# Kernel tuning notes

Hardware: AMD Instinct MI355X
Metric: run time of the kernel (lower is better)

The kernel has to match this reference:

```python
import jax, jax.numpy as jnp
import numpy as np

B, T, I, H, O = 256, 512, 128, 512, 64
ALPHA = 0.2          # cfg.leak
BETA = 8.0           # cfg.softplus_beta
THRESH = 20.0        # cfg.softplus_threshold


def _phi(x):
    # F.softplus(x, beta, threshold): linear when beta*x > threshold
    z = BETA * x
    return jnp.where(z > THRESH, x, jax.nn.softplus(jnp.minimum(z, THRESH)) / BETA)


def setup_inputs() -> dict:
    key = jax.random.key(0)
    ks = jax.random.split(key, 6)
    x = jax.random.normal(ks[0], (B, T, I), dtype=jnp.float32)
    W_xh = jax.random.normal(ks[1], (H, I), dtype=jnp.float32) * (1.0 / np.sqrt(I))
    # E/I structure: column-wise sign (abs weights * sign), scaled to modest spectral radius
    sign = np.ones(H, dtype=np.float32)
    perm = np.random.default_rng(0).permutation(H)
    sign[perm[int(round(0.8 * H)):]] = -1.0
    W_hh = jnp.abs(jax.random.normal(ks[2], (H, H), dtype=jnp.float32)) * jnp.asarray(sign)[None, :]
    W_hh = W_hh * (1.2 / (jnp.linalg.norm(W_hh, ord=2) + 1e-6))
    b_h = jnp.zeros((H,), dtype=jnp.float32)
    W_out = jax.random.normal(ks[3], (O, H), dtype=jnp.float32) * (1.0 / np.sqrt(H))
    b_out = jnp.zeros((O,), dtype=jnp.float32)
    return {"x": x, "W_xh": W_xh, "W_hh": W_hh, "b_h": b_h, "W_out": W_out, "b_out": b_out}


def reference(x, W_xh, W_hh, b_h, W_out, b_out):
    # precompute input projection: [B,T,H]
    xw = jnp.einsum('bti,hi->bth', x, W_xh)

    def step(h, xw_t):  # h: [B,H], xw_t: [B,H]
        pre = xw_t + h @ W_hh.T + b_h
        h = (1.0 - ALPHA) * h + ALPHA * _phi(pre)
        y = h @ W_out.T + b_out  # readout='all'
        return h, y

    h0 = jnp.zeros((x.shape[0], W_hh.shape[0]), dtype=x.dtype)
    _, ys = jax.lax.scan(step, h0, jnp.swapaxes(xw, 0, 1))  # ys: [T,B,O]
    return jnp.swapaxes(ys, 0, 1)  # [B,T,O]
```

## Files before the change

kernel.cpp:

```cpp
#include <hip/hip_runtime.h>


#define BB 256
#define TT 512
#define II 128
#define HH 512
#define OO 64
#define RG 16
#define JC 64
#define NG 16
#define NC 8
#define NB (NG * NC)

typedef _Float16 f16;
typedef f16 f16x8 __attribute__((ext_vector_type(8)));
typedef float f32x4 __attribute__((ext_vector_type(4)));

__global__ __launch_bounds__(256, 1)
void eirnn_persist(const float* __restrict__ x,
                   const float* __restrict__ Wxh,
                   const float* __restrict__ Whh,
                   const float* __restrict__ bh,
                   const float* __restrict__ Wout,
                   const float* __restrict__ bout,
                   float* __restrict__ yout,
                   unsigned long long* __restrict__ hbuf)
{
    const int tid  = threadIdx.x;
    const int bid  = blockIdx.x;
    const int wave = tid >> 6;
    const int lane = tid & 63;
    const int quad = lane >> 4;
    const int l16  = lane & 15;
    const int mm   = bid >> 3;
    const int c    = mm >> 1;
    const int r    = (bid & 7) * 2 + (mm & 1);
    const int rowbase = r * RG;
    const int jbase   = c * JC;
    const int myrow   = wave * 16 + l16;

    __shared__ __align__(16) f16 hg[2][RG][HH + 8];
    __shared__ __align__(16) f16 xsh[2][RG][II + 8];

    f16x8 bf[16];
    f16x8 xbf[4];
    f16x8 bfo[2];
    {
        const float* wp = Whh + (size_t)(jbase + myrow) * HH + quad * 8;
        #pragma unroll
        for (int ks = 0; ks < 16; ++ks) {
            float4 u = *(const float4*)(wp + ks * 32);
            float4 v = *(const float4*)(wp + ks * 32 + 4);
            f16x8 tv;
            tv[0]=(f16)u.x; tv[1]=(f16)u.y; tv[2]=(f16)u.z; tv[3]=(f16)u.w;
            tv[4]=(f16)v.x; tv[5]=(f16)v.y; tv[6]=(f16)v.z; tv[7]=(f16)v.w;
            bf[ks] = tv;
        }
        const float* wq = Wxh + (size_t)(jbase + myrow) * II + quad * 8;
        #pragma unroll
        for (int ks = 0; ks < 4; ++ks) {
            float4 u = *(const float4*)(wq + ks * 32);
            float4 v = *(const float4*)(wq + ks * 32 + 4);
            f16x8 tv;
            tv[0]=(f16)u.x; tv[1]=(f16)u.y; tv[2]=(f16)u.z; tv[3]=(f16)u.w;
            tv[4]=(f16)v.x; tv[5]=(f16)v.y; tv[6]=(f16)v.z; tv[7]=(f16)v.w;
            xbf[ks] = tv;
        }
        const float* wo = Wout + (size_t)myrow * HH + c * 64 + quad * 8;
        #pragma unroll
        for (int ks = 0; ks < 2; ++ks) {
            float4 u = *(const float4*)(wo + ks * 32);
            float4 v = *(const float4*)(wo + ks * 32 + 4);
            f16x8 tv;
            tv[0]=(f16)u.x; tv[1]=(f16)u.y; tv[2]=(f16)u.z; tv[3]=(f16)u.w;
            tv[4]=(f16)v.x; tv[5]=(f16)v.y; tv[6]=(f16)v.z; tv[7]=(f16)v.w;
            bfo[ks] = tv;
        }
    }
    const float biash = bh[jbase + myrow];
    const float biaso = (c == 0) ? bout[myrow] : 0.0f;

    for (int p = tid; p < RG * (HH + 8); p += 256)
        ((unsigned int*)hg)[p] = 0u;

    float hreg[4] = {0.f, 0.f, 0.f, 0.f};

    const int j8     = tid;
    const int gshard = j8 >> 5;

    float4 xpf0, xpf1;
    {
        int p0 = tid, p1 = tid + 256;
        xpf0 = ((const float4*)(x + ((size_t)(rowbase + (p0 >> 5)) * TT + 0) * II))[p0 & 31];
        xpf1 = ((const float4*)(x + ((size_t)(rowbase + (p1 >> 5)) * TT + 0) * II))[p1 & 31];
    }

    __syncthreads();

    for (int t = 0; t <= TT; ++t) {
        const int pcur = t & 1;

        if (t < TT) {
            int p0 = tid, p1 = tid + 256;
            f16* d0 = &xsh[pcur][p0 >> 5][(p0 & 31) * 4];
            d0[0]=(f16)xpf0.x; d0[1]=(f16)xpf0.y; d0[2]=(f16)xpf0.z; d0[3]=(f16)xpf0.w;
            f16* d1 = &xsh[pcur][p1 >> 5][(p1 & 31) * 4];
            d1[0]=(f16)xpf1.x; d1[1]=(f16)xpf1.y; d1[2]=(f16)xpf1.z; d1[3]=(f16)xpf1.w;
        }
        if (t + 1 < TT) {
            int p0 = tid, p1 = tid + 256;
            xpf0 = ((const float4*)(x + ((size_t)(rowbase + (p0 >> 5)) * TT + (t + 1)) * II))[p0 & 31];
            xpf1 = ((const float4*)(x + ((size_t)(rowbase + (p1 >> 5)) * TT + (t + 1)) * II))[p1 & 31];
        }
        if (t >= 1 && gshard != c) {
            const unsigned long long* src = hbuf
                + (size_t)pcur * (BB * HH / 2)
                + (size_t)rowbase * (HH / 2) + j8;
            const unsigned int tg = (unsigned)t;
            unsigned long long v0, v1, v2, v3, v4, v5, v6, v7;
            unsigned long long v8, v9, v10, v11, v12, v13, v14, v15;
            int round = 0;
            for (;;) {
                if ((round & 3) != 3) {
                    asm volatile(
                        "global_load_dwordx2 %0, %8, off sc0\n\t"
                        "global_load_dwordx2 %1, %9, off sc0\n\t"
                        "global_load_dwordx2 %2, %10, off sc0\n\t"
                        "global_load_dwordx2 %3, %11, off sc0\n\t"
                        "global_load_dwordx2 %4, %12, off sc0\n\t"
                        "global_load_dwordx2 %5, %13, off sc0\n\t"
                        "global_load_dwordx2 %6, %14, off sc0\n\t"
                        "global_load_dwordx2 %7, %15, off sc0"
                        : "=&v"(v0), "=&v"(v1), "=&v"(v2), "=&v"(v3),
                          "=&v"(v4), "=&v"(v5), "=&v"(v6), "=&v"(v7)
                        : "v"((unsigned long long)(src)),
                          "v"((unsigned long long)(src + 1 * (HH / 2))),
                          "v"((unsigned long long)(src + 2 * (HH / 2))),
                          "v"((unsigned long long)(src + 3 * (HH / 2))),
                          "v"((unsigned long long)(src + 4 * (HH / 2))),
                          "v"((unsigned long long)(src + 5 * (HH / 2))),
                          "v"((unsigned long long)(src + 6 * (HH / 2))),
                          "v"((unsigned long long)(src + 7 * (HH / 2))));
                    asm volatile(
                        "global_load_dwordx2 %0, %16, off sc0\n\t"
                        "global_load_dwordx2 %1, %17, off sc0\n\t"
                        "global_load_dwordx2 %2, %18, off sc0\n\t"
                        "global_load_dwordx2 %3, %19, off sc0\n\t"
                        "global_load_dwordx2 %4, %20, off sc0\n\t"
                        "global_load_dwordx2 %5, %21, off sc0\n\t"
                        "global_load_dwordx2 %6, %22, off sc0\n\t"
                        "global_load_dwordx2 %7, %23, off sc0\n\t"
                        "s_waitcnt vmcnt(0)"
                        : "=&v"(v8), "=&v"(v9), "=&v"(v10), "=&v"(v11),
                          "=&v"(v12), "=&v"(v13), "=&v"(v14), "=&v"(v15),
                          "+v"(v0), "+v"(v1), "+v"(v2), "+v"(v3),
                          "+v"(v4), "+v"(v5), "+v"(v6), "+v"(v7)
                        : "v"((unsigned long long)(src + 8 * (HH / 2))),
                          "v"((unsigned long long)(src + 9 * (HH / 2))),
                          "v"((unsigned long long)(src + 10 * (HH / 2))),
                          "v"((unsigned long long)(src + 11 * (HH / 2))),
                          "v"((unsigned long long)(src + 12 * (HH / 2))),
                          "v"((unsigned long long)(src + 13 * (HH / 2))),
                          "v"((unsigned long long)(src + 14 * (HH / 2))),
                          "v"((unsigned long long)(src + 15 * (HH / 2))));
                    __builtin_amdgcn_sched_barrier(0);
                } else {
                    v0  = __hip_atomic_load(src +  0 * (HH / 2), __ATOMIC_RELAXED, __HIP_MEMORY_SCOPE_AGENT);
                    v1  = __hip_atomic_load(src +  1 * (HH / 2), __ATOMIC_RELAXED, __HIP_MEMORY_SCOPE_AGENT);
                    v2  = __hip_atomic_load(src +  2 * (HH / 2), __ATOMIC_RELAXED, __HIP_MEMORY_SCOPE_AGENT);
                    v3  = __hip_atomic_load(src +  3 * (HH / 2), __ATOMIC_RELAXED, __HIP_MEMORY_SCOPE_AGENT);
                    v4  = __hip_atomic_load(src +  4 * (HH / 2), __ATOMIC_RELAXED, __HIP_MEMORY_SCOPE_AGENT);
                    v5  = __hip_atomic_load(src +  5 * (HH / 2), __ATOMIC_RELAXED, __HIP_MEMORY_SCOPE_AGENT);
                    v6  = __hip_atomic_load(src +  6 * (HH / 2), __ATOMIC_RELAXED, __HIP_MEMORY_SCOPE_AGENT);
                    v7  = __hip_atomic_load(src +  7 * (HH / 2), __ATOMIC_RELAXED, __HIP_MEMORY_SCOPE_AGENT);
                    v8  = __hip_atomic_load(src +  8 * (HH / 2), __ATOMIC_RELAXED, __HIP_MEMORY_SCOPE_AGENT);
                    v9  = __hip_atomic_load(src +  9 * (HH / 2), __ATOMIC_RELAXED, __HIP_MEMORY_SCOPE_AGENT);
                    v10 = __hip_atomic_load(src + 10 * (HH / 2), __ATOMIC_RELAXED, __HIP_MEMORY_SCOPE_AGENT);
                    v11 = __hip_atomic_load(src + 11 * (HH / 2), __ATOMIC_RELAXED, __HIP_MEMORY_SCOPE_AGENT);
                    v12 = __hip_atomic_load(src + 12 * (HH / 2), __ATOMIC_RELAXED, __HIP_MEMORY_SCOPE_AGENT);
                    v13 = __hip_atomic_load(src + 13 * (HH / 2), __ATOMIC_RELAXED, __HIP_MEMORY_SCOPE_AGENT);
                    v14 = __hip_atomic_load(src + 14 * (HH / 2), __ATOMIC_RELAXED, __HIP_MEMORY_SCOPE_AGENT);
                    v15 = __hip_atomic_load(src + 15 * (HH / 2), __ATOMIC_RELAXED, __HIP_MEMORY_SCOPE_AGENT);
                }
                bool ok = ((unsigned)(v0  >> 32) == tg) & ((unsigned)(v1  >> 32) == tg)
                        & ((unsigned)(v2  >> 32) == tg) & ((unsigned)(v3  >> 32) == tg)
                        & ((unsigned)(v4  >> 32) == tg) & ((unsigned)(v5  >> 32) == tg)
                        & ((unsigned)(v6  >> 32) == tg) & ((unsigned)(v7  >> 32) == tg)
                        & ((unsigned)(v8  >> 32) == tg) & ((unsigned)(v9  >> 32) == tg)
                        & ((unsigned)(v10 >> 32) == tg) & ((unsigned)(v11 >> 32) == tg)
                        & ((unsigned)(v12 >> 32) == tg) & ((unsigned)(v13 >> 32) == tg)
                        & ((unsigned)(v14 >> 32) == tg) & ((unsigned)(v15 >> 32) == tg);
                if (ok) break;
                ++round;
            }
            *(unsigned int*)&hg[pcur][ 0][j8 * 2] = (unsigned int)v0;
            *(unsigned int*)&hg[pcur][ 1][j8 * 2] = (unsigned int)v1;
            *(unsigned int*)&hg[pcur][ 2][j8 * 2] = (unsigned int)v2;
            *(unsigned int*)&hg[pcur][ 3][j8 * 2] = (unsigned int)v3;
            *(unsigned int*)&hg[pcur][ 4][j8 * 2] = (unsigned int)v4;
            *(unsigned int*)&hg[pcur][ 5][j8 * 2] = (unsigned int)v5;
            *(unsigned int*)&hg[pcur][ 6][j8 * 2] = (unsigned int)v6;
            *(unsigned int*)&hg[pcur][ 7][j8 * 2] = (unsigned int)v7;
            *(unsigned int*)&hg[pcur][ 8][j8 * 2] = (unsigned int)v8;
            *(unsigned int*)&hg[pcur][ 9][j8 * 2] = (unsigned int)v9;
            *(unsigned int*)&hg[pcur][10][j8 * 2] = (unsigned int)v10;
            *(unsigned int*)&hg[pcur][11][j8 * 2] = (unsigned int)v11;
            *(unsigned int*)&hg[pcur][12][j8 * 2] = (unsigned int)v12;
            *(unsigned int*)&hg[pcur][13][j8 * 2] = (unsigned int)v13;
            *(unsigned int*)&hg[pcur][14][j8 * 2] = (unsigned int)v14;
            *(unsigned int*)&hg[pcur][15][j8 * 2] = (unsigned int)v15;
        }
        __syncthreads();

        if (t < TT) {
            f32x4 acc0 = {0.f,0.f,0.f,0.f}, acc1 = {0.f,0.f,0.f,0.f};
            #pragma unroll
            for (int ks = 0; ks < 16; ks += 2) {
                f16x8 a0 = *(const f16x8*)&hg[pcur][l16][ks * 32 + quad * 8];
                f16x8 a1 = *(const f16x8*)&hg[pcur][l16][(ks + 1) * 32 + quad * 8];
                acc0 = __builtin_amdgcn_mfma_f32_16x16x32_f16(a0, bf[ks], acc0, 0, 0, 0);
                acc1 = __builtin_amdgcn_mfma_f32_16x16x32_f16(a1, bf[ks + 1], acc1, 0, 0, 0);
            }
            #pragma unroll
            for (int ks = 0; ks < 4; ks += 2) {
                f16x8 a0 = *(const f16x8*)&xsh[pcur][l16][ks * 32 + quad * 8];
                f16x8 a1 = *(const f16x8*)&xsh[pcur][l16][(ks + 1) * 32 + quad * 8];
                acc0 = __builtin_amdgcn_mfma_f32_16x16x32_f16(a0, xbf[ks], acc0, 0, 0, 0);
                acc1 = __builtin_amdgcn_mfma_f32_16x16x32_f16(a1, xbf[ks + 1], acc1, 0, 0, 0);
            }
            unsigned long long* dst64 = hbuf + (size_t)((t + 1) & 1) * (BB * HH / 2);
            const unsigned long long tagw = ((unsigned long long)(unsigned)(t + 1)) << 32;
            unsigned int hb[4];
            #pragma unroll
            for (int reg = 0; reg < 4; ++reg) {
                float pre = acc0[reg] + acc1[reg] + biash;
                float z = 8.f * pre;
                float ph = (z > 20.f) ? pre : (__logf(1.f + __expf(z)) * 0.125f);
                float hn = 0.8f * hreg[reg] + 0.2f * ph;
                hreg[reg] = hn;
                hb[reg] = (unsigned int)__builtin_bit_cast(unsigned short, (f16)hn);
            }
            #pragma unroll
            for (int reg = 0; reg < 4; ++reg) {
                unsigned int ob = (unsigned int)__shfl_xor((int)hb[reg], 1, 64);
                if ((lane & 1) == 0) {
                    unsigned int pair = hb[reg] | (ob << 16);
                    size_t eidx = (size_t)(rowbase + quad * 4 + reg) * HH + jbase + myrow;
                    __hip_atomic_store(dst64 + (eidx >> 1), tagw | (unsigned long long)pair,
                                       __ATOMIC_RELAXED, __HIP_MEMORY_SCOPE_AGENT);
                    *(unsigned int*)&hg[(t + 1) & 1][quad * 4 + reg][jbase + myrow] = pair;
                }
            }
        }

        if (t >= 1) {
            f32x4 ya = {0.f,0.f,0.f,0.f};
            f16x8 a0 = *(const f16x8*)&hg[pcur][l16][c * 64 + quad * 8];
            f16x8 a1 = *(const f16x8*)&hg[pcur][l16][c * 64 + 32 + quad * 8];
            ya = __builtin_amdgcn_mfma_f32_16x16x32_f16(a0, bfo[0], ya, 0, 0, 0);
            ya = __builtin_amdgcn_mfma_f32_16x16x32_f16(a1, bfo[1], ya, 0, 0, 0);
            #pragma unroll
            for (int reg = 0; reg < 4; ++reg)
                atomicAdd(yout + ((size_t)(rowbase + quad * 4 + reg) * TT + (t - 1)) * OO + myrow,
                          ya[reg] + biaso);
        }
    }
}

extern "C" void kernel_launch(void* const* d_in, const int* in_sizes, int n_in,
                              void* d_out, int out_size, void* d_ws, size_t ws_size,
                              hipStream_t stream)
{
    const float* x    = (const float*)d_in[0];
    const float* Wxh  = (const float*)d_in[1];
    const float* Whh  = (const float*)d_in[2];
    const float* bh   = (const float*)d_in[3];
    const float* Wout = (const float*)d_in[4];
    const float* bout = (const float*)d_in[5];
    float* yout = (float*)d_out;

    unsigned long long* hbuf = (unsigned long long*)d_ws;
    const size_t hbuf_bytes = (size_t)2 * BB * (HH / 2) * sizeof(unsigned long long);

    if (ws_size < hbuf_bytes) return;

    hipMemsetAsync(hbuf, 0, hbuf_bytes, stream);
    hipMemsetAsync(yout, 0, (size_t)out_size * sizeof(float), stream);

    eirnn_persist<<<dim3(NB), dim3(256), 0, stream>>>(
        x, Wxh, Whh, bh, Wout, bout, yout, hbuf);
}
```

Measured before the change: 1.370 ms.

## Compute full readout in column-block 0 and replace atomic adds with plain stores

The output projection used to be split across all 8 column blocks, each adding a partial 64-wide sum into y with float atomics. Now only the c==0 blocks compute the full 512-wide readout, reusing the h fragments already loaded for the recurrent MFMA, and write y with plain stores. This removes per-step global atomics and the need for y to be pre-zeroed. The cost is 16 more f16x8 weight registers per thread, extra MFMAs on the c==0 blocks, and load imbalance that could stretch the critical path of the lockstep recurrence.

```diff
diff --git a/kernel.cpp b/kernel.cpp
--- a/kernel.cpp
+++ b/kernel.cpp
@@ -44,7 +44,7 @@
 
     f16x8 bf[16];
     f16x8 xbf[4];
-    f16x8 bfo[2];
+    f16x8 bfo2[16];
     {
         const float* wp = Whh + (size_t)(jbase + myrow) * HH + quad * 8;
         #pragma unroll
@@ -66,19 +66,19 @@
             tv[4]=(f16)v.x; tv[5]=(f16)v.y; tv[6]=(f16)v.z; tv[7]=(f16)v.w;
             xbf[ks] = tv;
         }
-        const float* wo = Wout + (size_t)myrow * HH + c * 64 + quad * 8;
+        const float* wo = Wout + (size_t)myrow * HH + quad * 8;
         #pragma unroll
-        for (int ks = 0; ks < 2; ++ks) {
+        for (int ks = 0; ks < 16; ++ks) {
             float4 u = *(const float4*)(wo + ks * 32);
             float4 v = *(const float4*)(wo + ks * 32 + 4);
             f16x8 tv;
             tv[0]=(f16)u.x; tv[1]=(f16)u.y; tv[2]=(f16)u.z; tv[3]=(f16)u.w;
             tv[4]=(f16)v.x; tv[5]=(f16)v.y; tv[6]=(f16)v.z; tv[7]=(f16)v.w;
-            bfo[ks] = tv;
+            bfo2[ks] = tv;
         }
     }
     const float biash = bh[jbase + myrow];
-    const float biaso = (c == 0) ? bout[myrow] : 0.0f;
+    const float biaso = bout[myrow];
 
     for (int p = tid; p < RG * (HH + 8); p += 256)
         ((unsigned int*)hg)[p] = 0u;
@@ -213,13 +213,19 @@
         __syncthreads();
 
         if (t < TT) {
+            const bool dordo = (c == 0) && (t >= 1);
             f32x4 acc0 = {0.f,0.f,0.f,0.f}, acc1 = {0.f,0.f,0.f,0.f};
+            f32x4 ya   = {0.f,0.f,0.f,0.f};
             #pragma unroll
             for (int ks = 0; ks < 16; ks += 2) {
                 f16x8 a0 = *(const f16x8*)&hg[pcur][l16][ks * 32 + quad * 8];
                 f16x8 a1 = *(const f16x8*)&hg[pcur][l16][(ks + 1) * 32 + quad * 8];
                 acc0 = __builtin_amdgcn_mfma_f32_16x16x32_f16(a0, bf[ks], acc0, 0, 0, 0);
                 acc1 = __builtin_amdgcn_mfma_f32_16x16x32_f16(a1, bf[ks + 1], acc1, 0, 0, 0);
+                if (dordo) {
+                    ya = __builtin_amdgcn_mfma_f32_16x16x32_f16(a0, bfo2[ks], ya, 0, 0, 0);
+                    ya = __builtin_amdgcn_mfma_f32_16x16x32_f16(a1, bfo2[ks + 1], ya, 0, 0, 0);
+                }
             }
             #pragma unroll
             for (int ks = 0; ks < 4; ks += 2) {
@@ -251,18 +257,23 @@
                     *(unsigned int*)&hg[(t + 1) & 1][quad * 4 + reg][jbase + myrow] = pair;
                 }
             }
-        }
-
-        if (t >= 1) {
+            if (dordo) {
+                #pragma unroll
+                for (int reg = 0; reg < 4; ++reg)
+                    yout[((size_t)(rowbase + quad * 4 + reg) * TT + (t - 1)) * OO + myrow]
+                        = ya[reg] + biaso;
+            }
+        } else if (c == 0) {
             f32x4 ya = {0.f,0.f,0.f,0.f};
-            f16x8 a0 = *(const f16x8*)&hg[pcur][l16][c * 64 + quad * 8];
-            f16x8 a1 = *(const f16x8*)&hg[pcur][l16][c * 64 + 32 + quad * 8];
-            ya = __builtin_amdgcn_mfma_f32_16x16x32_f16(a0, bfo[0], ya, 0, 0, 0);
-            ya = __builtin_amdgcn_mfma_f32_16x16x32_f16(a1, bfo[1], ya, 0, 0, 0);
+            #pragma unroll
+            for (int ks = 0; ks < 16; ++ks) {
+                f16x8 a0 = *(const f16x8*)&hg[pcur][l16][ks * 32 + quad * 8];
+                ya = __builtin_amdgcn_mfma_f32_16x16x32_f16(a0, bfo2[ks], ya, 0, 0, 0);
+            }
             #pragma unroll
             for (int reg = 0; reg < 4; ++reg)
-                atomicAdd(yout + ((size_t)(rowbase + quad * 4 + reg) * TT + (t - 1)) * OO + myrow,
-                          ya[reg] + biaso);
+                yout[((size_t)(rowbase + quad * 4 + reg) * TT + (TT - 1)) * OO + myrow]
+                    = ya[reg] + biaso;
         }
     }
 }
```

Result: slower. 1.400 ms (+2.2%).
